# Performance work log

Hardware: AMD Instinct MI355X
Metric: run time of the kernel (lower is better)

Reference implementation:

```python
import jax, jax.numpy as jnp
import numpy as np
from jax import lax

# Dims: B=batch, Cin=in_channel, Ch=channel (bottleneck), Br=breadth (num expert kernels)
B, Cin, Ch, Br, H, W = 16, 256, 128, 8, 64, 64


def setup_inputs() -> dict:
    key = jax.random.key(0)
    ks = jax.random.split(key, 6)
    sc = lambda k, shape: jax.random.normal(k, shape, jnp.float32) * 0.05
    return {
        "x": jax.random.normal(ks[0], (B, Cin, H, W), jnp.float32),
        # SwitchedConv #1: 3x3, in_channel -> channel, breadth expert kernels
        "W1": sc(ks[1], (Br, Ch, Cin, 3, 3)),
        "b1": jnp.zeros((Ch,), jnp.float32),
        # lambda coupler #1: 1x1 projection in_channel -> breadth (per-pixel routing)
        "Wc1": sc(ks[2], (Br, Cin)),
        "bc1": jnp.zeros((Br,), jnp.float32),
        # SwitchedConv #2: 1x1, channel -> in_channel
        "W2": sc(ks[3], (Br, Cin, Ch, 1, 1)),
        "b2": jnp.zeros((Cin,), jnp.float32),
        # lambda coupler #2: 1x1 projection channel -> breadth
        "Wc2": sc(ks[4], (Br, Ch)),
        "bc2": jnp.zeros((Br,), jnp.float32),
    }


def _switched_conv(x, Wk, b, Wc, bc, pad):
    """Input-conditioned mixture of `breadth` conv kernels.

    The coupler (1x1 projection of x to breadth logits, softmax over breadth)
    produces per-pixel mixture weights; each expert kernel's conv output is
    combined per-pixel with these weights.
    x: [B, Cin, H, W]; Wk: [Br, Cout, Cin, k, k]
    """
    br, cout, cin, k, _ = Wk.shape
    bsz, _, h, w = x.shape
    # per-pixel routing weights over the breadth dim: [B, Br, H, W]
    sel = jax.nn.softmax(jnp.einsum('bihw,gi->bghw', x, Wc) + bc[None, :, None, None], axis=1)
    # all breadth branches in one grouped-output conv: [B, Br*Cout, H, W]
    y = lax.conv_general_dilated(
        x, Wk.reshape(br * cout, cin, k, k),
        window_strides=(1, 1), padding=[(pad, pad), (pad, pad)],
        dimension_numbers=('NCHW', 'OIHW', 'NCHW'))
    y = y.reshape(bsz, br, cout, h, w)
    # selection-weighted reduction over breadth + bias
    return jnp.einsum('bgchw,bghw->bchw', y, sel) + b[None, :, None, None]


def reference(x, W1, b1, Wc1, bc1, W2, b2, Wc2, bc2):
    h = jax.nn.relu(x)
    h = _switched_conv(h, W1, b1, Wc1, bc1, pad=1)  # 3x3 switched conv
    h = jax.nn.relu(h)
    h = _switched_conv(h, W2, b2, Wc2, bc2, pad=0)  # 1x1 switched conv
    return h + x  # residual add
```

## Files before the change

kernel.cpp:

```cpp
#include <hip/hip_runtime.h>
#include <hip/hip_bf16.h>
#include <cstdint>

typedef _Float16 h8 __attribute__((ext_vector_type(8)));
typedef _Float16 h4 __attribute__((ext_vector_type(4)));
typedef float    f4 __attribute__((ext_vector_type(4)));
typedef float    fx16 __attribute__((ext_vector_type(16)));


#define GLD16(src, dst) __builtin_amdgcn_global_load_lds( \
    (const __attribute__((address_space(1))) void*)(src), \
    (__attribute__((address_space(3))) void*)(dst), 16, 0, 0)

__global__ __launch_bounds__(256) void prep_w_k(const float* __restrict__ W1,
        const float* __restrict__ W2, _Float16* __restrict__ W1r,
        _Float16* __restrict__ W2r) {
    int i = blockIdx.x * 256 + threadIdx.x;
    if (i < 2359296) {
        int g = i / 294912;  int r  = i - g * 294912;
        int c = r / 2304;    int r2 = r - c * 2304;
        int ci = r2 / 9;     int tap = r2 - ci * 9;
        int s = (ci & 31) >> 3;
        int pos = (s ^ ((c >> 1) & 3)) * 8 + (ci & 7);
        W1r[(((size_t)(ci >> 5) * 9 + tap) * 32768)
            + g * 4096 + c * 32 + pos] = (_Float16)W1[i];
    } else {
        int i2 = i - 2359296;
        int g = i2 >> 15; int r = i2 & 32767; int co = r >> 7; int ch = r & 127;
        W2r[(((size_t)g * 4 + (ch >> 5)) * 256 + co) * 32 + (ch & 31)]
            = (_Float16)W2[i2];
    }
}

__global__ __launch_bounds__(256) void prep_x_k(const float* __restrict__ x,
        const float* __restrict__ Wc1, const float* __restrict__ bc1,
        float* __restrict__ sel1) {
    __shared__ float wc[2048];
    int t = threadIdx.x;
    for (int i = t; i < 2048; i += 256) wc[i] = Wc1[i];
    __syncthreads();
    int pix = blockIdx.x * 256 + t;
    int b = pix >> 12, p = pix & 4095;
    const float* xp = x + (size_t)b * 1048576 + p;
    float lg[8] = {0.f,0.f,0.f,0.f,0.f,0.f,0.f,0.f};
    for (int c = 0; c < 256; ++c) {
        float v = fmaxf(xp[(size_t)c * 4096], 0.f);
        #pragma unroll
        for (int g = 0; g < 8; ++g) lg[g] += wc[g * 256 + c] * v;
    }
    float m = -1e30f;
    #pragma unroll
    for (int g = 0; g < 8; ++g) { lg[g] += bc1[g]; m = fmaxf(m, lg[g]); }
    float sum = 0.f;
    #pragma unroll
    for (int g = 0; g < 8; ++g) { lg[g] = __expf(lg[g] - m); sum += lg[g]; }
    float inv = 1.f / sum;
    #pragma unroll
    for (int g = 0; g < 8; ++g)
        sel1[(size_t)(b * 8 + g) * 4096 + p] = lg[g] * inv;
}

__global__ __launch_bounds__(512, 2) void conv1_k(const float* __restrict__ x,
        const _Float16* __restrict__ W1r, const float* __restrict__ sel1,
        const float* __restrict__ b1, _Float16* __restrict__ hr) {
    __shared__ _Float16 wt[2][32768];
    __shared__ _Float16 xs[12296];
    int t = threadIdx.x;
    int b = blockIdx.y, yt = blockIdx.x;
    int y0 = yt * 4;
    int w = t >> 6, l = t & 63;
    int wm = w >> 2, wn = w & 3;
    int l31 = l & 31, kq2 = l >> 5;
    if (t < 8) xs[12288 + t] = (_Float16)0.f;

    fx16 acc[2][2];
    #pragma unroll
    for (int m = 0; m < 2; ++m)
        #pragma unroll
        for (int n = 0; n < 2; ++n)
            #pragma unroll
            for (int e = 0; e < 16; ++e) acc[m][n][e] = 0.f;

    {
        const _Float16* srcw = W1r + (size_t)t * 8;
        _Float16* dw = wt[0] + t * 8;
        #pragma unroll
        for (int it = 0; it < 8; ++it)
            GLD16(srcw + it * 4096, dw + it * 4096);
    }

    int px[2];
    #pragma unroll
    for (int nf = 0; nf < 2; ++nf) px[nf] = wn * 64 + nf * 32 + l31;
    bool e0 = (l31 == 0), e63 = (l31 == 31);
    int afo[2][2];
    #pragma unroll
    for (int m = 0; m < 2; ++m)
        #pragma unroll
        for (int kc = 0; kc < 2; ++kc) {
            int c = wm * 64 + m * 32 + l31;
            afo[m][kc] = c * 32 + (((kc * 2 + kq2) ^ ((c >> 1) & 3)) * 8);
        }
    int ba[2][3][2];
    #pragma unroll
    for (int nf = 0; nf < 2; ++nf)
        #pragma unroll
        for (int kx = 0; kx < 3; ++kx) {
            int rz = px[nf] + kx - 1;
            #pragma unroll
            for (int kc = 0; kc < 2; ++kc)
                ba[nf][kx][kc] = rz * 32 + (((kc * 2 + kq2) ^ ((rz >> 1) & 3)) * 8);
        }
    h8 selv[2];
    #pragma unroll
    for (int nf = 0; nf < 2; ++nf)
        #pragma unroll
        for (int g = 0; g < 8; ++g)
            selv[nf][g] = (_Float16)sel1[(size_t)(b * 8 + g) * 4096 + yt * 256 + px[nf]];

    #pragma unroll 1
    for (int ci = 0; ci < 8; ++ci) {
        __syncthreads();
        if (t < 384) {
            int r = t >> 6, col = t & 63;
            int rc = r * 64 + col;
            int yi = y0 - 1 + r;
            _Float16* dx = xs + rc * 32;
            int rx = (rc >> 1) & 3;
            if (yi >= 0 && yi < 64) {
                const float* xp = x + ((size_t)(b * 256 + ci * 32)) * 4096 + yi * 64 + col;
                float v[32];
                #pragma unroll
                for (int c2 = 0; c2 < 32; ++c2)
                    v[c2] = fmaxf(xp[(size_t)c2 * 4096], 0.f);
                #pragma unroll
                for (int qq = 0; qq < 4; ++qq) {
                    h8 hv;
                    #pragma unroll
                    for (int e = 0; e < 8; ++e) hv[e] = (_Float16)v[qq * 8 + e];
                    *(h8*)(dx + (qq ^ rx) * 8) = hv;
                }
            } else {
                const h8 HZ = {};
                #pragma unroll
                for (int qq = 0; qq < 4; ++qq)
                    *(h8*)(dx + (qq ^ rx) * 8) = HZ;
            }
        }
        #pragma unroll 1
        for (int ky = 0; ky < 3; ++ky) {
            #pragma unroll
            for (int kx = 0; kx < 3; ++kx) {
                int grp = ci * 9 + ky * 3 + kx;
                __syncthreads();
                if (grp < 71) {
                    const _Float16* srcw = W1r + (size_t)(grp + 1) * 32768 + t * 8;
                    _Float16* dw = wt[(grp + 1) & 1] + t * 8;
                    #pragma unroll
                    for (int it = 0; it < 8; ++it)
                        GLD16(srcw + it * 4096, dw + it * 4096);
                }
                h8 bfr[2][2];
                #pragma unroll
                for (int nf = 0; nf < 2; ++nf)
                    #pragma unroll
                    for (int kc = 0; kc < 2; ++kc) {
                        int a = ba[nf][kx][kc] + ky * 2048;
                        if (kx == 0 && nf == 0) a = e0 ? 12288 : a;
                        if (kx == 2 && nf == 1) a = e63 ? 12288 : a;
                        bfr[nf][kc] = *(const h8*)(xs + a);
                    }
                const _Float16* wp = wt[grp & 1];
                #pragma unroll
                for (int g = 0; g < 8; ++g) {
                    h8 a00 = *(const h8*)(wp + g * 4096 + afo[0][0]);
                    h8 a01 = *(const h8*)(wp + g * 4096 + afo[0][1]);
                    h8 a10 = *(const h8*)(wp + g * 4096 + afo[1][0]);
                    h8 a11 = *(const h8*)(wp + g * 4096 + afo[1][1]);
                    #pragma unroll
                    for (int nf = 0; nf < 2; ++nf) {
                        _Float16 sg = selv[nf][g];
                        h8 b0 = bfr[nf][0] * sg;
                        h8 b1v = bfr[nf][1] * sg;
                        acc[0][nf] = __builtin_amdgcn_mfma_f32_32x32x16_f16(
                            a00, b0, acc[0][nf], 0, 0, 0);
                        acc[1][nf] = __builtin_amdgcn_mfma_f32_32x32x16_f16(
                            a10, b0, acc[1][nf], 0, 0, 0);
                        acc[0][nf] = __builtin_amdgcn_mfma_f32_32x32x16_f16(
                            a01, b1v, acc[0][nf], 0, 0, 0);
                        acc[1][nf] = __builtin_amdgcn_mfma_f32_32x32x16_f16(
                            a11, b1v, acc[1][nf], 0, 0, 0);
                    }
                }
            }
        }
    }
    #pragma unroll
    for (int m = 0; m < 2; ++m)
        #pragma unroll
        for (int nf = 0; nf < 2; ++nf) {
            size_t pg = ((size_t)(b * 4096 + yt * 256 + px[nf])) * 128;
            #pragma unroll
            for (int q = 0; q < 4; ++q) {
                int c0 = wm * 64 + m * 32 + q * 8 + kq2 * 4;
                f4 bb = *(const f4*)(b1 + c0);
                h4 hv;
                #pragma unroll
                for (int r = 0; r < 4; ++r)
                    hv[r] = (_Float16)fmaxf(acc[m][nf][q * 4 + r] + bb[r], 0.f);
                *(h4*)(hr + pg + c0) = hv;
            }
        }
}

__global__ __launch_bounds__(256) void sel2_k(const _Float16* __restrict__ hr,
        const float* __restrict__ Wc2, const float* __restrict__ bc2,
        float* __restrict__ sel2) {
    __shared__ float wc[1024];
    int t = threadIdx.x;
    for (int i = t; i < 1024; i += 256) wc[i] = Wc2[i];
    __syncthreads();
    int pix = blockIdx.x * 256 + t;
    const h8* hp = (const h8*)(hr + (size_t)pix * 128);
    float lg[8] = {0.f,0.f,0.f,0.f,0.f,0.f,0.f,0.f};
    for (int j = 0; j < 16; ++j) {
        h8 v = hp[j];
        #pragma unroll
        for (int e = 0; e < 8; ++e) {
            float f = (float)v[e];
            int c = j * 8 + e;
            #pragma unroll
            for (int g = 0; g < 8; ++g) lg[g] += wc[g * 128 + c] * f;
        }
    }
    float m = -1e30f;
    #pragma unroll
    for (int g = 0; g < 8; ++g) { lg[g] += bc2[g]; m = fmaxf(m, lg[g]); }
    float sum = 0.f;
    #pragma unroll
    for (int g = 0; g < 8; ++g) { lg[g] = __expf(lg[g] - m); sum += lg[g]; }
    float inv = 1.f / sum;
    int b = pix >> 12, p = pix & 4095;
    #pragma unroll
    for (int g = 0; g < 8; ++g)
        sel2[(size_t)(b * 8 + g) * 4096 + p] = lg[g] * inv;
}

__global__ __launch_bounds__(256, 2) void conv2_k(const _Float16* __restrict__ hr,
        const _Float16* __restrict__ W2r, const float* __restrict__ sel2,
        const float* __restrict__ b2, const float* __restrict__ x,
        float* __restrict__ out) {
    __shared__ _Float16 hs[64 * 128];
    __shared__ _Float16 wt[2][256 * 32];
    int t = threadIdx.x;
    int bid = blockIdx.x;
    int b = bid >> 6, p0 = (bid & 63) * 64;
    int l = t & 63, w = t >> 6;
    int wm = w >> 1, wn = w & 1;
    int l15 = l & 15, sl = l >> 4;
    int swl = (l15 & 7) << 3;
    const f4 FZ = {0.f, 0.f, 0.f, 0.f};
    f4 acce[8][2], accf[8][2];
    #pragma unroll
    for (int m = 0; m < 8; ++m)
        #pragma unroll
        for (int n = 0; n < 2; ++n) { acce[m][n] = FZ; accf[m][n] = FZ; }
    {
        int px = t >> 2, qq = t & 3;
        const _Float16* src = hr + (size_t)(b * 4096 + p0 + px) * 128 + qq * 32;
        #pragma unroll
        for (int u = 0; u < 4; ++u)
            *(h8*)(hs + ((px * 128 + qq * 32 + u * 8) ^ ((px & 7) << 3)))
                = *(const h8*)(src + u * 8);
    }
    float selr[8][2];
    #pragma unroll
    for (int g = 0; g < 8; ++g)
        #pragma unroll
        for (int n = 0; n < 2; ++n)
            selr[g][n] = sel2[(size_t)(b * 8 + g) * 4096 + p0 + wn * 32 + n * 16 + l15];
    int afo[8];
    #pragma unroll
    for (int m = 0; m < 8; ++m) {
        int c = wm * 128 + m * 16 + l15;
        afo[m] = ((c * 32 + sl * 8) ^ swl);
    }
    h8 wr[4];
    auto load_w = [&](int T) {
        const _Float16* srcw = W2r + (size_t)T * 8192;
        #pragma unroll
        for (int it = 0; it < 4; ++it)
            wr[it] = *(const h8*)(srcw + (size_t)(it * 256 + t) * 8);
    };
    auto write_w = [&](int bf) {
        #pragma unroll
        for (int it = 0; it < 4; ++it) {
            int cc = it * 256 + t;
            int c = cc >> 2, q = cc & 3;
            *(h8*)(wt[bf] + ((c * 32 + q * 8) ^ ((c & 7) << 3))) = wr[it];
        }
    };
    load_w(0);
    write_w(0);
    int buf = 0;
    #pragma unroll 1
    for (int T = 0; T < 32; ++T) {
        bool hn = (T < 31);
        if (hn) load_w(T + 1);
        __syncthreads();
        int kc = (T & 3) * 32;
        h8 bfv[2];
        #pragma unroll
        for (int n = 0; n < 2; ++n) {
            int px = wn * 32 + n * 16 + l15;
            bfv[n] = *(const h8*)(hs + ((px * 128 + kc + sl * 8) ^ ((px & 7) << 3)));
        }
        #pragma unroll
        for (int m = 0; m < 8; ++m) {
            h8 af = *(const h8*)(wt[buf] + afo[m]);
            #pragma unroll
            for (int n = 0; n < 2; ++n)
                acce[m][n] = __builtin_amdgcn_mfma_f32_16x16x32_f16(
                    af, bfv[n], acce[m][n], 0, 0, 0);
        }
        if ((T & 3) == 3) {
            int g = T >> 2;
            #pragma unroll
            for (int n = 0; n < 2; ++n)
                #pragma unroll
                for (int m = 0; m < 8; ++m) {
                    accf[m][n] += selr[g][n] * acce[m][n];
                    acce[m][n] = FZ;
                }
        }
        if (hn) write_w(buf ^ 1);
        buf ^= 1;
    }
    #pragma unroll
    for (int m = 0; m < 8; ++m) {
        int c0 = wm * 128 + m * 16 + sl * 4;
        f4 bb = *(const f4*)(b2 + c0);
        #pragma unroll
        for (int n = 0; n < 2; ++n) {
            int px = wn * 32 + n * 16 + l15;
            size_t o = (size_t)(b * 256 + c0) * 4096 + p0 + px;
            #pragma unroll
            for (int r = 0; r < 4; ++r)
                out[o + (size_t)r * 4096] = accf[m][n][r] + bb[r] + x[o + (size_t)r * 4096];
        }
    }
}

extern "C" void kernel_launch(void* const* d_in, const int* in_sizes, int n_in,
                              void* d_out, int out_size, void* d_ws, size_t ws_size,
                              hipStream_t stream) {
    const float* x   = (const float*)d_in[0];
    const float* W1  = (const float*)d_in[1];
    const float* b1  = (const float*)d_in[2];
    const float* Wc1 = (const float*)d_in[3];
    const float* bc1 = (const float*)d_in[4];
    const float* W2  = (const float*)d_in[5];
    const float* b2  = (const float*)d_in[6];
    const float* Wc2 = (const float*)d_in[7];
    const float* bc2 = (const float*)d_in[8];
    float* out = (float*)d_out;
    char* ws = (char*)d_ws;
    _Float16* hr  = (_Float16*)(ws);
    _Float16* W1r = (_Float16*)(ws + 16777216);
    _Float16* W2r = (_Float16*)(ws + 21495808);
    float* sel1   = (float*)(ws + 22020096);
    float* sel2   = (float*)(ws + 24117248);

    hipLaunchKernelGGL(prep_w_k, dim3(10240), dim3(256), 0, stream, W1, W2, W1r, W2r);
    hipLaunchKernelGGL(prep_x_k, dim3(256), dim3(256), 0, stream, x, Wc1, bc1, sel1);
    hipLaunchKernelGGL(conv1_k, dim3(16, 16), dim3(512), 0, stream, x, W1r, sel1, b1, hr);
    hipLaunchKernelGGL(sel2_k, dim3(256), dim3(256), 0, stream, hr, Wc2, bc2, sel2);
    hipLaunchKernelGGL(conv2_k, dim3(1024), dim3(256), 0, stream, hr, W2r, sel2, b2, x, out);
}
```

Measured before the change: 354.9 us.

## Shrink conv1 tiles to 2 rows and split weight staging into quarter chunks

The conv1 kernel moves from 512-thread blocks covering 4 output rows to 256-thread blocks covering 2 rows, doubling the grid. The weight stream is double-buffered in 8K-element chunks (two experts each) instead of 32K, so LDS per block falls from about 155KB to about 49KB and more blocks can be resident per CU. The cost is twice as many barriers per tap, weights re-streamed by twice as many blocks, and more halo-row traffic from x per block.

Measured after the change: 369.6 us. 1.04x slower.

```diff
diff --git a/kernel.cpp b/kernel.cpp
--- a/kernel.cpp
+++ b/kernel.cpp
@@ -60,18 +60,18 @@
         sel1[(size_t)(b * 8 + g) * 4096 + p] = lg[g] * inv;
 }
 
-__global__ __launch_bounds__(512, 2) void conv1_k(const float* __restrict__ x,
+__global__ __launch_bounds__(256, 2) void conv1_k(const float* __restrict__ x,
         const _Float16* __restrict__ W1r, const float* __restrict__ sel1,
         const float* __restrict__ b1, _Float16* __restrict__ hr) {
-    __shared__ _Float16 wt[2][32768];
-    __shared__ _Float16 xs[12296];
+    __shared__ _Float16 wt[2][8192];
+    __shared__ _Float16 xs[8224];
     int t = threadIdx.x;
     int b = blockIdx.y, yt = blockIdx.x;
-    int y0 = yt * 4;
+    int y0 = yt * 2;
     int w = t >> 6, l = t & 63;
-    int wm = w >> 2, wn = w & 3;
+    int wm = w >> 1, wn = w & 1;
     int l31 = l & 31, kq2 = l >> 5;
-    if (t < 8) xs[12288 + t] = (_Float16)0.f;
+    if (t < 32) xs[8192 + t] = (_Float16)0.f;
 
     fx16 acc[2][2];
     #pragma unroll
@@ -81,13 +81,13 @@
             #pragma unroll
             for (int e = 0; e < 16; ++e) acc[m][n][e] = 0.f;
 
-    {
-        const _Float16* srcw = W1r + (size_t)t * 8;
-        _Float16* dw = wt[0] + t * 8;
-        #pragma unroll
-        for (int it = 0; it < 8; ++it)
-            GLD16(srcw + it * 4096, dw + it * 4096);
-    }
+    auto stage_w = [&](int P, _Float16* dwb) {
+        const _Float16* srcw = W1r + (size_t)P * 8192 + t * 8;
+        _Float16* dw = dwb + t * 8;
+        #pragma unroll
+        for (int it = 0; it < 4; ++it)
+            GLD16(srcw + it * 2048, dw + it * 2048);
+    };
 
     int px[2];
     #pragma unroll
@@ -116,12 +116,13 @@
     for (int nf = 0; nf < 2; ++nf)
         #pragma unroll
         for (int g = 0; g < 8; ++g)
-            selv[nf][g] = (_Float16)sel1[(size_t)(b * 8 + g) * 4096 + yt * 256 + px[nf]];
-
+            selv[nf][g] = (_Float16)sel1[(size_t)(b * 8 + g) * 4096 + yt * 128 + px[nf]];
+
+    stage_w(0, wt[0]);
     #pragma unroll 1
     for (int ci = 0; ci < 8; ++ci) {
         __syncthreads();
-        if (t < 384) {
+        {
             int r = t >> 6, col = t & 63;
             int rc = r * 64 + col;
             int yi = y0 - 1 + r;
@@ -151,45 +152,39 @@
         for (int ky = 0; ky < 3; ++ky) {
             #pragma unroll
             for (int kx = 0; kx < 3; ++kx) {
-                int grp = ci * 9 + ky * 3 + kx;
-                __syncthreads();
-                if (grp < 71) {
-                    const _Float16* srcw = W1r + (size_t)(grp + 1) * 32768 + t * 8;
-                    _Float16* dw = wt[(grp + 1) & 1] + t * 8;
+                h8 bfr[2][2];
+                #pragma unroll
+                for (int gq = 0; gq < 4; ++gq) {
+                    int P = (ci * 9 + ky * 3 + kx) * 4 + gq;
+                    __syncthreads();
+                    if (P < 287) stage_w(P + 1, wt[(gq + 1) & 1]);
+                    if (gq == 0) {
+                        #pragma unroll
+                        for (int nf = 0; nf < 2; ++nf)
+                            #pragma unroll
+                            for (int kc = 0; kc < 2; ++kc) {
+                                int a = ba[nf][kx][kc] + ky * 2048;
+                                if (kx == 0 && nf == 0) a = e0 ? 8192 : a;
+                                if (kx == 2 && nf == 1) a = e63 ? 8192 : a;
+                                bfr[nf][kc] = *(const h8*)(xs + a);
+                            }
+                    }
+                    const _Float16* wp = wt[gq & 1];
                     #pragma unroll
-                    for (int it = 0; it < 8; ++it)
-                        GLD16(srcw + it * 4096, dw + it * 4096);
-                }
-                h8 bfr[2][2];
-                #pragma unroll
-                for (int nf = 0; nf < 2; ++nf)
-                    #pragma unroll
-                    for (int kc = 0; kc < 2; ++kc) {
-                        int a = ba[nf][kx][kc] + ky * 2048;
-                        if (kx == 0 && nf == 0) a = e0 ? 12288 : a;
-                        if (kx == 2 && nf == 1) a = e63 ? 12288 : a;
-                        bfr[nf][kc] = *(const h8*)(xs + a);
-                    }
-                const _Float16* wp = wt[grp & 1];
-                #pragma unroll
-                for (int g = 0; g < 8; ++g) {
-                    h8 a00 = *(const h8*)(wp + g * 4096 + afo[0][0]);
-                    h8 a01 = *(const h8*)(wp + g * 4096 + afo[0][1]);
-                    h8 a10 = *(const h8*)(wp + g * 4096 + afo[1][0]);
-                    h8 a11 = *(const h8*)(wp + g * 4096 + afo[1][1]);
-                    #pragma unroll
-                    for (int nf = 0; nf < 2; ++nf) {
-                        _Float16 sg = selv[nf][g];
-                        h8 b0 = bfr[nf][0] * sg;
-                        h8 b1v = bfr[nf][1] * sg;
-                        acc[0][nf] = __builtin_amdgcn_mfma_f32_32x32x16_f16(
-                            a00, b0, acc[0][nf], 0, 0, 0);
-                        acc[1][nf] = __builtin_amdgcn_mfma_f32_32x32x16_f16(
-                            a10, b0, acc[1][nf], 0, 0, 0);
-                        acc[0][nf] = __builtin_amdgcn_mfma_f32_32x32x16_f16(
-                            a01, b1v, acc[0][nf], 0, 0, 0);
-                        acc[1][nf] = __builtin_amdgcn_mfma_f32_32x32x16_f16(
-                            a11, b1v, acc[1][nf], 0, 0, 0);
+                    for (int gl = 0; gl < 2; ++gl) {
+                        #pragma unroll
+                        for (int kc = 0; kc < 2; ++kc) {
+                            h8 a0 = *(const h8*)(wp + gl * 4096 + afo[0][kc]);
+                            h8 a1 = *(const h8*)(wp + gl * 4096 + afo[1][kc]);
+                            #pragma unroll
+                            for (int nf = 0; nf < 2; ++nf) {
+                                h8 bs = bfr[nf][kc] * selv[nf][gq * 2 + gl];
+                                acc[0][nf] = __builtin_amdgcn_mfma_f32_32x32x16_f16(
+                                    a0, bs, acc[0][nf], 0, 0, 0);
+                                acc[1][nf] = __builtin_amdgcn_mfma_f32_32x32x16_f16(
+                                    a1, bs, acc[1][nf], 0, 0, 0);
+                            }
+                        }
                     }
                 }
             }
@@ -199,7 +194,7 @@
     for (int m = 0; m < 2; ++m)
         #pragma unroll
         for (int nf = 0; nf < 2; ++nf) {
-            size_t pg = ((size_t)(b * 4096 + yt * 256 + px[nf])) * 128;
+            size_t pg = ((size_t)(b * 4096 + yt * 128 + px[nf])) * 128;
             #pragma unroll
             for (int q = 0; q < 4; ++q) {
                 int c0 = wm * 64 + m * 32 + q * 8 + kq2 * 4;
@@ -373,7 +368,7 @@
 
     hipLaunchKernelGGL(prep_w_k, dim3(10240), dim3(256), 0, stream, W1, W2, W1r, W2r);
     hipLaunchKernelGGL(prep_x_k, dim3(256), dim3(256), 0, stream, x, Wc1, bc1, sel1);
-    hipLaunchKernelGGL(conv1_k, dim3(16, 16), dim3(512), 0, stream, x, W1r, sel1, b1, hr);
+    hipLaunchKernelGGL(conv1_k, dim3(32, 16), dim3(256), 0, stream, x, W1r, sel1, b1, hr);
     hipLaunchKernelGGL(sel2_k, dim3(256), dim3(256), 0, stream, hr, Wc2, bc2, sel2);
     hipLaunchKernelGGL(conv2_k, dim3(1024), dim3(256), 0, stream, hr, W2r, sel2, b2, x, out);
 }
```

## Fuse second coupler softmax into conv2 and vectorize weight prep writes

Applied to the files above, without the earlier changes.

Removes the separate sel2 kernel: conv2 now computes the per-pixel routing logits and softmax from its shared-memory copy of the hidden tile, reducing partial sums across four threads per pixel through shared memory. The weight-prep kernel is rewritten so each thread gathers eight source elements and writes one contiguous 16-byte fp16 vector, with 8x fewer blocks. This drops a kernel launch and a global round trip of hr and sel2, but adds about 14KB of LDS per conv2 block and extra barriers, which may reduce occupancy.

After: 348.0 us. No clear change (-1.9%).

```diff
diff --git a/kernel.cpp b/kernel.cpp
--- a/kernel.cpp
+++ b/kernel.cpp
@@ -15,20 +15,31 @@
 __global__ __launch_bounds__(256) void prep_w_k(const float* __restrict__ W1,
         const float* __restrict__ W2, _Float16* __restrict__ W1r,
         _Float16* __restrict__ W2r) {
-    int i = blockIdx.x * 256 + threadIdx.x;
-    if (i < 2359296) {
-        int g = i / 294912;  int r  = i - g * 294912;
-        int c = r / 2304;    int r2 = r - c * 2304;
-        int ci = r2 / 9;     int tap = r2 - ci * 9;
-        int s = (ci & 31) >> 3;
-        int pos = (s ^ ((c >> 1) & 3)) * 8 + (ci & 7);
-        W1r[(((size_t)(ci >> 5) * 9 + tap) * 32768)
-            + g * 4096 + c * 32 + pos] = (_Float16)W1[i];
+    int o8 = blockIdx.x * 256 + threadIdx.x;
+    if (o8 < 294912) {
+        int sq = o8 & 3;
+        int c  = (o8 >> 2) & 127;
+        int g  = (o8 >> 9) & 7;
+        int tk = o8 >> 12;
+        int tap = tk % 9, cik = tk / 9;
+        int s = sq ^ ((c >> 1) & 3);
+        int ci0 = cik * 32 + s * 8;
+        const float* src = W1 + ((size_t)(g * 128 + c) * 256 + ci0) * 9 + tap;
+        h8 v;
+        #pragma unroll
+        for (int e = 0; e < 8; ++e) v[e] = (_Float16)src[e * 9];
+        *(h8*)(W1r + (size_t)o8 * 8) = v;
     } else {
-        int i2 = i - 2359296;
-        int g = i2 >> 15; int r = i2 & 32767; int co = r >> 7; int ch = r & 127;
-        W2r[(((size_t)g * 4 + (ch >> 5)) * 256 + co) * 32 + (ch & 31)]
-            = (_Float16)W2[i2];
+        int ow = o8 - 294912;
+        int sg = ow & 3;
+        int co = (ow >> 2) & 255;
+        int kc = (ow >> 10) & 3;
+        int g  = ow >> 12;
+        const float* src = W2 + ((size_t)(g * 256 + co) * 128) + kc * 32 + sg * 8;
+        h8 v;
+        #pragma unroll
+        for (int e = 0; e < 8; ++e) v[e] = (_Float16)src[e];
+        *(h8*)(W2r + (size_t)ow * 8) = v;
     }
 }
 
@@ -213,45 +224,15 @@
         }
 }
 
-__global__ __launch_bounds__(256) void sel2_k(const _Float16* __restrict__ hr,
-        const float* __restrict__ Wc2, const float* __restrict__ bc2,
-        float* __restrict__ sel2) {
-    __shared__ float wc[1024];
-    int t = threadIdx.x;
-    for (int i = t; i < 1024; i += 256) wc[i] = Wc2[i];
-    __syncthreads();
-    int pix = blockIdx.x * 256 + t;
-    const h8* hp = (const h8*)(hr + (size_t)pix * 128);
-    float lg[8] = {0.f,0.f,0.f,0.f,0.f,0.f,0.f,0.f};
-    for (int j = 0; j < 16; ++j) {
-        h8 v = hp[j];
-        #pragma unroll
-        for (int e = 0; e < 8; ++e) {
-            float f = (float)v[e];
-            int c = j * 8 + e;
-            #pragma unroll
-            for (int g = 0; g < 8; ++g) lg[g] += wc[g * 128 + c] * f;
-        }
-    }
-    float m = -1e30f;
-    #pragma unroll
-    for (int g = 0; g < 8; ++g) { lg[g] += bc2[g]; m = fmaxf(m, lg[g]); }
-    float sum = 0.f;
-    #pragma unroll
-    for (int g = 0; g < 8; ++g) { lg[g] = __expf(lg[g] - m); sum += lg[g]; }
-    float inv = 1.f / sum;
-    int b = pix >> 12, p = pix & 4095;
-    #pragma unroll
-    for (int g = 0; g < 8; ++g)
-        sel2[(size_t)(b * 8 + g) * 4096 + p] = lg[g] * inv;
-}
-
 __global__ __launch_bounds__(256, 2) void conv2_k(const _Float16* __restrict__ hr,
-        const _Float16* __restrict__ W2r, const float* __restrict__ sel2,
-        const float* __restrict__ b2, const float* __restrict__ x,
-        float* __restrict__ out) {
+        const _Float16* __restrict__ W2r, const float* __restrict__ Wc2,
+        const float* __restrict__ bc2, const float* __restrict__ b2,
+        const float* __restrict__ x, float* __restrict__ out) {
     __shared__ _Float16 hs[64 * 128];
     __shared__ _Float16 wt[2][256 * 32];
+    __shared__ float wc[1024];
+    __shared__ float red[2048];
+    __shared__ float selw[512];
     int t = threadIdx.x;
     int bid = blockIdx.x;
     int b = bid >> 6, p0 = (bid & 63) * 64;
@@ -265,6 +246,7 @@
     for (int m = 0; m < 8; ++m)
         #pragma unroll
         for (int n = 0; n < 2; ++n) { acce[m][n] = FZ; accf[m][n] = FZ; }
+    for (int i = t; i < 1024; i += 256) wc[i] = Wc2[i];
     {
         int px = t >> 2, qq = t & 3;
         const _Float16* src = hr + (size_t)(b * 4096 + p0 + px) * 128 + qq * 32;
@@ -272,18 +254,6 @@
         for (int u = 0; u < 4; ++u)
             *(h8*)(hs + ((px * 128 + qq * 32 + u * 8) ^ ((px & 7) << 3)))
                 = *(const h8*)(src + u * 8);
-    }
-    float selr[8][2];
-    #pragma unroll
-    for (int g = 0; g < 8; ++g)
-        #pragma unroll
-        for (int n = 0; n < 2; ++n)
-            selr[g][n] = sel2[(size_t)(b * 8 + g) * 4096 + p0 + wn * 32 + n * 16 + l15];
-    int afo[8];
-    #pragma unroll
-    for (int m = 0; m < 8; ++m) {
-        int c = wm * 128 + m * 16 + l15;
-        afo[m] = ((c * 32 + sl * 8) ^ swl);
     }
     h8 wr[4];
     auto load_w = [&](int T) {
@@ -301,7 +271,54 @@
         }
     };
     load_w(0);
+    __syncthreads();
+    {
+        int px = t >> 2, qq = t & 3;
+        float lg[8] = {0.f,0.f,0.f,0.f,0.f,0.f,0.f,0.f};
+        #pragma unroll
+        for (int u = 0; u < 4; ++u) {
+            h8 v = *(const h8*)(hs + ((px * 128 + qq * 32 + u * 8) ^ ((px & 7) << 3)));
+            #pragma unroll
+            for (int e = 0; e < 8; ++e) {
+                float f = (float)v[e];
+                int c = qq * 32 + u * 8 + e;
+                #pragma unroll
+                for (int g = 0; g < 8; ++g) lg[g] += wc[g * 128 + c] * f;
+            }
+        }
+        #pragma unroll
+        for (int g = 0; g < 8; ++g) red[(px * 8 + g) * 4 + qq] = lg[g];
+    }
+    __syncthreads();
+    if (t < 64) {
+        float lg[8]; float m = -1e30f;
+        #pragma unroll
+        for (int g = 0; g < 8; ++g) {
+            lg[g] = red[(t*8+g)*4+0] + red[(t*8+g)*4+1]
+                  + red[(t*8+g)*4+2] + red[(t*8+g)*4+3] + bc2[g];
+            m = fmaxf(m, lg[g]);
+        }
+        float sum = 0.f;
+        #pragma unroll
+        for (int g = 0; g < 8; ++g) { lg[g] = __expf(lg[g] - m); sum += lg[g]; }
+        float inv = 1.f / sum;
+        #pragma unroll
+        for (int g = 0; g < 8; ++g) selw[t * 8 + g] = lg[g] * inv;
+    }
     write_w(0);
+    __syncthreads();
+    float selr[8][2];
+    #pragma unroll
+    for (int g = 0; g < 8; ++g)
+        #pragma unroll
+        for (int n = 0; n < 2; ++n)
+            selr[g][n] = selw[(wn * 32 + n * 16 + l15) * 8 + g];
+    int afo[8];
+    #pragma unroll
+    for (int m = 0; m < 8; ++m) {
+        int c = wm * 128 + m * 16 + l15;
+        afo[m] = ((c * 32 + sl * 8) ^ swl);
+    }
     int buf = 0;
     #pragma unroll 1
     for (int T = 0; T < 32; ++T) {
@@ -369,11 +386,9 @@
     _Float16* W1r = (_Float16*)(ws + 16777216);
     _Float16* W2r = (_Float16*)(ws + 21495808);
     float* sel1   = (float*)(ws + 22020096);
-    float* sel2   = (float*)(ws + 24117248);
-
-    hipLaunchKernelGGL(prep_w_k, dim3(10240), dim3(256), 0, stream, W1, W2, W1r, W2r);
+
+    hipLaunchKernelGGL(prep_w_k, dim3(1280), dim3(256), 0, stream, W1, W2, W1r, W2r);
     hipLaunchKernelGGL(prep_x_k, dim3(256), dim3(256), 0, stream, x, Wc1, bc1, sel1);
     hipLaunchKernelGGL(conv1_k, dim3(16, 16), dim3(512), 0, stream, x, W1r, sel1, b1, hr);
-    hipLaunchKernelGGL(sel2_k, dim3(256), dim3(256), 0, stream, hr, Wc2, bc2, sel2);
-    hipLaunchKernelGGL(conv2_k, dim3(1024), dim3(256), 0, stream, hr, W2r, sel2, b2, x, out);
-}
+    hipLaunchKernelGGL(conv2_k, dim3(1024), dim3(256), 0, stream, hr, W2r, Wc2, bc2, b2, x, out);
+}
```
